# Optimization experiments

Hardware: AMD Instinct MI355X
Metric: run time of the kernel (lower is better)

Reference implementation:

```python
import jax, jax.numpy as jnp
import numpy as np

B, D, H = 65536, 64, 512  # batch, input_dim (even), hidden_dim; num_layers=4 -> 4 Linears


def setup_inputs() -> dict:
    key = jax.random.key(0)
    ks = jax.random.split(key, 10)
    s_in = 1.0 / np.sqrt(D)
    s_h = 1.0 / np.sqrt(H)
    return {
        "t": jnp.zeros((1,), jnp.float32),
        "x": jax.random.normal(ks[0], (B, D), jnp.float32),
        "W0": jax.random.uniform(ks[1], (D, H), jnp.float32, -s_in, s_in),
        "b0": jax.random.uniform(ks[2], (H,), jnp.float32, -s_in, s_in),
        "W1": jax.random.uniform(ks[3], (H, H), jnp.float32, -s_h, s_h),
        "b1": jax.random.uniform(ks[4], (H,), jnp.float32, -s_h, s_h),
        "W2": jax.random.uniform(ks[5], (H, H), jnp.float32, -s_h, s_h),
        "b2": jax.random.uniform(ks[6], (H,), jnp.float32, -s_h, s_h),
        "W3": jax.random.uniform(ks[7], (H, 1), jnp.float32, -s_h, s_h),
        "b3": jax.random.uniform(ks[8], (1,), jnp.float32, -s_h, s_h),
    }


def reference(t, x, W0, b0, W1, b1, W2, b2, W3, b3):
    # Hamiltonian MLP: Linear->Tanh x3, final Linear to scalar energy per sample.
    def hamiltonian_sum(xx):
        h = jnp.tanh(xx @ W0 + b0)
        h = jnp.tanh(h @ W1 + b1)
        h = jnp.tanh(h @ W2 + b2)
        return jnp.sum(h @ W3 + b3)

    gradH = jax.grad(hamiltonian_sum)(x)  # [B, D]
    n = D // 2
    # gradH @ J.T with symplectic J == concat(gradH_p, -gradH_q)
    return jnp.concatenate([gradH[:, n:], -gradH[:, :n]], axis=1)
```

## Files before the change

### kernel.cpp

```cpp
#include <hip/hip_runtime.h>
#include <hip/hip_bf16.h>

typedef unsigned short u16;
typedef short s16x8 __attribute__((ext_vector_type(8)));
typedef float f32x4 __attribute__((ext_vector_type(4)));

#define MFMA_BF16(a, b, c) __builtin_amdgcn_mfma_f32_16x16x32_bf16((a), (b), (c), 0, 0, 0)

static constexpr int D_IN   = 64;
static constexpr int H_DIM  = 512;
static constexpr int M_TILE = 64;
static constexpr int AST    = 520;
static constexpr int XST    = 72;

__device__ __forceinline__ u16 f2bf(float f) {
  unsigned u = __builtin_bit_cast(unsigned, f);
  u += 0x7fffu + ((u >> 16) & 1u);
  return (u16)(u >> 16);
}
__device__ __forceinline__ float bfb2f(unsigned bits16) {
  return __builtin_bit_cast(float, bits16 << 16);
}
__device__ __forceinline__ float fast_tanh(float x) {
  float e = __expf(2.0f * x);
  return 1.0f - 2.0f * __builtin_amdgcn_rcpf(e + 1.0f);
}
#if defined(__gfx950__) && __has_builtin(__builtin_amdgcn_cvt_pk_bf16_f32)
__device__ __forceinline__ unsigned pk2bf(float a, float b) {
  typedef __bf16 bf16x2_t __attribute__((ext_vector_type(2)));
  bf16x2_t v = __builtin_amdgcn_cvt_pk_bf16_f32(a, b);
  return __builtin_bit_cast(unsigned, v);
}
#else
__device__ __forceinline__ unsigned pk2bf(float a, float b) {
  return (unsigned)f2bf(a) | ((unsigned)f2bf(b) << 16);
}
#endif

__global__ void prep_weights(const float* __restrict__ W0,
                             const float* __restrict__ W1,
                             const float* __restrict__ W2,
                             const float* __restrict__ W3,
                             u16* __restrict__ ws) {
  u16* p0f = ws;
  u16* p0b = p0f + D_IN * H_DIM;
  u16* p1f = p0b + D_IN * H_DIM;
  u16* p1b = p1f + H_DIM * H_DIM;
  u16* p2f = p1b + H_DIM * H_DIM;
  u16* p2b = p2f + H_DIM * H_DIM;

  int t = blockIdx.x * 256 + threadIdx.x;
  int lane = t & 63;
  int kc   = (t >> 6) & 15;
  int ntg  = t >> 10;
  int ln = lane & 15, q = lane >> 4;
  int n = ntg * 16 + ln;
  int k = kc * 32 + q * 8;

  #pragma unroll
  for (int j = 0; j < 8; ++j) {
    p1f[t * 8 + j] = f2bf(W1[(k + j) * 512 + n]);
    p2f[t * 8 + j] = f2bf(W2[(k + j) * 512 + n]);
    p1b[t * 8 + j] = f2bf(W1[n * 512 + (k + j)]);
    p2b[t * 8 + j] = f2bf(W2[n * 512 + (k + j)] * W3[k + j]);
  }
  if (kc < 2) {
    int t0 = (ntg * 2 + kc) * 64 + lane;
    #pragma unroll
    for (int j = 0; j < 8; ++j)
      p0f[t0 * 8 + j] = f2bf(W0[(k + j) * 512 + n]);
  }
  if (ntg < 4) {
    int t0 = (ntg * 16 + kc) * 64 + lane;
    #pragma unroll
    for (int j = 0; j < 8; ++j)
      p0b[t0 * 8 + j] = f2bf(W0[n * 512 + (k + j)]);
  }
}

#define LOAD_W4(BP, KC, WA)                                                     \
  {                                                                             \
    const u16* _sr = (BP) + ((size_t)wave << 15) + ((KC) << 9) + lane * 8;      \
    _Pragma("unroll")                                                           \
    for (int s = 0; s < 4; ++s)                                                 \
      (WA)[s] = *(const s16x8*)(_sr + (s << 13));                               \
  }
#define WA_PROLOGUE2(BP)                                                        \
  { LOAD_W4(BP, 0, wa0); LOAD_W4(BP, 1, wa1); }

#define STEP2(KC, WA, BP)                                                       \
  {                                                                             \
    s16x8 b[4];                                                                 \
    _Pragma("unroll")                                                           \
    for (int nt = 0; nt < 4; ++nt)                                              \
      b[nt] = *(const s16x8*)(buf + (nt * 16 + ln) * AST + (KC) * 32 + q * 8);  \
    _Pragma("unroll")                                                           \
    for (int nt = 0; nt < 4; ++nt)                                              \
      _Pragma("unroll")                                                         \
      for (int mt = 0; mt < 4; ++mt)                                            \
        acc[mt][nt] = MFMA_BF16((WA)[mt], b[nt], acc[mt][nt]);                  \
    if ((KC) + 2 < 16) LOAD_W4(BP, (KC) + 2, WA);                               \
  }

#define GEMM512_REG(BP)                                                         \
  {                                                                             \
    STEP2( 0, wa0, BP); STEP2( 1, wa1, BP);                                     \
    STEP2( 2, wa0, BP); STEP2( 3, wa1, BP);                                     \
    STEP2( 4, wa0, BP); STEP2( 5, wa1, BP);                                     \
    STEP2( 6, wa0, BP); STEP2( 7, wa1, BP);                                     \
    STEP2( 8, wa0, BP); STEP2( 9, wa1, BP);                                     \
    STEP2(10, wa0, BP); STEP2(11, wa1, BP);                                     \
    STEP2(12, wa0, BP); STEP2(13, wa1, BP);                                     \
    STEP2(14, wa0, BP); STEP2(15, wa1, BP);                                     \
  }

#define ACC_INIT_BIAS(BIAS)                                                     \
  {                                                                             \
    _Pragma("unroll")                                                           \
    for (int mt = 0; mt < 4; ++mt) {                                            \
      float4 bv = *(const float4*)((BIAS) + wave * 64 + mt * 16 + q * 4);       \
      _Pragma("unroll")                                                         \
      for (int nt = 0; nt < 4; ++nt)                                            \
        acc[mt][nt] = (f32x4){bv.x, bv.y, bv.z, bv.w};                          \
    }                                                                           \
  }
#define ACC_INIT_ZERO()                                                         \
  {                                                                             \
    _Pragma("unroll") for (int mt = 0; mt < 4; ++mt)                            \
      _Pragma("unroll") for (int nt = 0; nt < 4; ++nt)                          \
        acc[mt][nt] = (f32x4){0.f, 0.f, 0.f, 0.f};                              \
  }

__global__ __launch_bounds__(512, 2) void hnn_fused(
    const float* __restrict__ x,
    const float* __restrict__ bias0,
    const float* __restrict__ bias1,
    const float* __restrict__ bias2,
    const u16* __restrict__ ws,
    float* __restrict__ out)
{
  const u16* p0f = ws;
  const u16* p0b = p0f + D_IN * H_DIM;
  const u16* p1f = p0b + D_IN * H_DIM;
  const u16* p1b = p1f + H_DIM * H_DIM;
  const u16* p2f = p1b + H_DIM * H_DIM;
  const u16* p2b = p2f + H_DIM * H_DIM;

  __shared__ __align__(16) u16 xs[M_TILE * XST];
  __shared__ __align__(16) u16 buf[M_TILE * AST];

  const int tid  = threadIdx.x;
  const int wave = tid >> 6;
  const int lane = tid & 63;
  const int ln   = lane & 15;
  const int q    = lane >> 4;
  const int m0   = wave * 64;
  const int row0 = blockIdx.x * M_TILE;

  {
    int r = tid >> 3, c = (tid & 7) * 8;
    const float4* src = (const float4*)(x + (size_t)(row0 + r) * D_IN + c);
    float4 f0 = src[0];
    float4 f1 = src[1];
    u16* dst = xs + r * XST + c;
    dst[0] = f2bf(f0.x); dst[1] = f2bf(f0.y); dst[2] = f2bf(f0.z); dst[3] = f2bf(f0.w);
    dst[4] = f2bf(f1.x); dst[5] = f2bf(f1.y); dst[6] = f2bf(f1.z); dst[7] = f2bf(f1.w);
  }
  __syncthreads();

  f32x4 acc[4][4];
  s16x8 wa0[4], wa1[4];
  unsigned h0p[4][4][2];
  unsigned h1p[4][4][2];

  ACC_INIT_BIAS(bias0);
  {
    const u16* ap0 = p0f + (wave << 12) + lane * 8;
    #pragma unroll
    for (int kc = 0; kc < 2; ++kc) {
      s16x8 b[4];
      #pragma unroll
      for (int nt = 0; nt < 4; ++nt)
        b[nt] = *(const s16x8*)(xs + (nt * 16 + ln) * XST + kc * 32 + q * 8);
      #pragma unroll
      for (int mt = 0; mt < 4; ++mt) {
        s16x8 a = *(const s16x8*)(ap0 + (mt << 10) + (kc << 9));
        #pragma unroll
        for (int nt = 0; nt < 4; ++nt)
          acc[mt][nt] = MFMA_BF16(a, b[nt], acc[mt][nt]);
      }
    }
  }
  WA_PROLOGUE2(p1f);
  #pragma unroll
  for (int mt = 0; mt < 4; ++mt)
    #pragma unroll
    for (int nt = 0; nt < 4; ++nt) {
      unsigned p01 = pk2bf(fast_tanh(acc[mt][nt][0]), fast_tanh(acc[mt][nt][1]));
      unsigned p23 = pk2bf(fast_tanh(acc[mt][nt][2]), fast_tanh(acc[mt][nt][3]));
      h0p[mt][nt][0] = p01; h0p[mt][nt][1] = p23;
      *(uint2*)(buf + (nt * 16 + ln) * AST + m0 + mt * 16 + q * 4) =
          make_uint2(p01, p23);
    }
  __syncthreads();

  ACC_INIT_BIAS(bias1);
  GEMM512_REG(p1f);
  __syncthreads();
  WA_PROLOGUE2(p2f);
  #pragma unroll
  for (int mt = 0; mt < 4; ++mt)
    #pragma unroll
    for (int nt = 0; nt < 4; ++nt) {
      unsigned p01 = pk2bf(fast_tanh(acc[mt][nt][0]), fast_tanh(acc[mt][nt][1]));
      unsigned p23 = pk2bf(fast_tanh(acc[mt][nt][2]), fast_tanh(acc[mt][nt][3]));
      h1p[mt][nt][0] = p01; h1p[mt][nt][1] = p23;
      *(uint2*)(buf + (nt * 16 + ln) * AST + m0 + mt * 16 + q * 4) =
          make_uint2(p01, p23);
    }
  __syncthreads();

  ACC_INIT_BIAS(bias2);
  GEMM512_REG(p2f);
  __syncthreads();
  WA_PROLOGUE2(p2b);
  #pragma unroll
  for (int mt = 0; mt < 4; ++mt)
    #pragma unroll
    for (int nt = 0; nt < 4; ++nt) {
      float t0 = fast_tanh(acc[mt][nt][0]), t1 = fast_tanh(acc[mt][nt][1]);
      float t2 = fast_tanh(acc[mt][nt][2]), t3 = fast_tanh(acc[mt][nt][3]);
      unsigned p01 = pk2bf(1.0f - t0 * t0, 1.0f - t1 * t1);
      unsigned p23 = pk2bf(1.0f - t2 * t2, 1.0f - t3 * t3);
      *(uint2*)(buf + (nt * 16 + ln) * AST + m0 + mt * 16 + q * 4) =
          make_uint2(p01, p23);
    }
  __syncthreads();

  ACC_INIT_ZERO();
  GEMM512_REG(p2b);
  __syncthreads();
  WA_PROLOGUE2(p1b);
  #pragma unroll
  for (int mt = 0; mt < 4; ++mt)
    #pragma unroll
    for (int nt = 0; nt < 4; ++nt) {
      unsigned pa = h1p[mt][nt][0], pb = h1p[mt][nt][1];
      float h0v = bfb2f(pa & 0xffffu), h1v = bfb2f(pa >> 16);
      float h2v = bfb2f(pb & 0xffffu), h3v = bfb2f(pb >> 16);
      unsigned p01 = pk2bf(acc[mt][nt][0] * (1.0f - h0v * h0v),
                           acc[mt][nt][1] * (1.0f - h1v * h1v));
      unsigned p23 = pk2bf(acc[mt][nt][2] * (1.0f - h2v * h2v),
                           acc[mt][nt][3] * (1.0f - h3v * h3v));
      *(uint2*)(buf + (nt * 16 + ln) * AST + m0 + mt * 16 + q * 4) =
          make_uint2(p01, p23);
    }
  __syncthreads();

  ACC_INIT_ZERO();
  GEMM512_REG(p1b);
  __syncthreads();
  #pragma unroll
  for (int mt = 0; mt < 4; ++mt)
    #pragma unroll
    for (int nt = 0; nt < 4; ++nt) {
      unsigned pa = h0p[mt][nt][0], pb = h0p[mt][nt][1];
      float h0v = bfb2f(pa & 0xffffu), h1v = bfb2f(pa >> 16);
      float h2v = bfb2f(pb & 0xffffu), h3v = bfb2f(pb >> 16);
      unsigned p01 = pk2bf(acc[mt][nt][0] * (1.0f - h0v * h0v),
                           acc[mt][nt][1] * (1.0f - h1v * h1v));
      unsigned p23 = pk2bf(acc[mt][nt][2] * (1.0f - h2v * h2v),
                           acc[mt][nt][3] * (1.0f - h3v * h3v));
      *(uint2*)(buf + (nt * 16 + ln) * AST + m0 + mt * 16 + q * 4) =
          make_uint2(p01, p23);
    }
  __syncthreads();

  {
    f32x4 acc5[2];
    acc5[0] = (f32x4){0.f, 0.f, 0.f, 0.f};
    acc5[1] = (f32x4){0.f, 0.f, 0.f, 0.f};
    const int mt5 = wave & 3;
    const int n0  = (wave >> 2) * 32;
    const u16* ap5 = p0b + (mt5 << 13) + lane * 8;
    #pragma unroll 2
    for (int kc = 0; kc < 16; ++kc) {
      s16x8 a = *(const s16x8*)(ap5 + (kc << 9));
      #pragma unroll
      for (int nt = 0; nt < 2; ++nt) {
        s16x8 b = *(const s16x8*)(buf + (n0 + nt * 16 + ln) * AST + kc * 32 + q * 8);
        acc5[nt] = MFMA_BF16(a, b, acc5[nt]);
      }
    }
    int g0 = mt5 * 16 + q * 4;
    int c0 = (g0 < 32) ? g0 + 32 : g0 - 32;
    float s = (g0 < 32) ? -1.0f : 1.0f;
    #pragma unroll
    for (int nt = 0; nt < 2; ++nt) {
      int smp = row0 + n0 + nt * 16 + ln;
      float4 v = make_float4(s * acc5[nt][0], s * acc5[nt][1],
                             s * acc5[nt][2], s * acc5[nt][3]);
      *(float4*)(out + (size_t)smp * 64 + c0) = v;
    }
  }
}

extern "C" void kernel_launch(void* const* d_in, const int* in_sizes, int n_in,
                              void* d_out, int out_size, void* d_ws, size_t ws_size,
                              hipStream_t stream) {
  const float* x  = (const float*)d_in[1];
  const float* W0 = (const float*)d_in[2];
  const float* b0 = (const float*)d_in[3];
  const float* W1 = (const float*)d_in[4];
  const float* b1 = (const float*)d_in[5];
  const float* W2 = (const float*)d_in[6];
  const float* b2 = (const float*)d_in[7];
  const float* W3 = (const float*)d_in[8];
  u16* ws = (u16*)d_ws;
  float* out = (float*)d_out;

  prep_weights<<<128, 256, 0, stream>>>(W0, W1, W2, W3, ws);
  hnn_fused<<<65536 / M_TILE, 512, 0, stream>>>(x, b0, b1, b2, ws, out);
}
```

Before: 244.6 us.

## Double-buffer LDS activations to drop post-GEMM barriers and keep h1 in LDS

The single shared activation buffer becomes two ping-pong LDS buffers. Each layer's epilogue writes into the buffer the just-finished GEMM was not reading, so the __syncthreads after every 512-wide GEMM is removed. The h1 activations are no longer held in registers; they stay in the second LDS buffer and are read back and overwritten in place during the backward step, freeing about 32 VGPRs per thread. The cost is roughly 66 KB more LDS per block, which likely leaves room for only one 512-thread block per CU instead of the two requested by the launch bounds.

Result: faster. 229.2 us (-6.3%).

```diff
diff --git a/kernel.cpp b/kernel.cpp
--- a/kernel.cpp
+++ b/kernel.cpp
@@ -88,12 +88,12 @@
 #define WA_PROLOGUE2(BP)                                                        \
   { LOAD_W4(BP, 0, wa0); LOAD_W4(BP, 1, wa1); }
 
-#define STEP2(KC, WA, BP)                                                       \
+#define STEP2(KC, WA, BP, BUF)                                                  \
   {                                                                             \
     s16x8 b[4];                                                                 \
     _Pragma("unroll")                                                           \
     for (int nt = 0; nt < 4; ++nt)                                              \
-      b[nt] = *(const s16x8*)(buf + (nt * 16 + ln) * AST + (KC) * 32 + q * 8);  \
+      b[nt] = *(const s16x8*)((BUF) + (nt * 16 + ln) * AST + (KC) * 32 + q * 8);\
     _Pragma("unroll")                                                           \
     for (int nt = 0; nt < 4; ++nt)                                              \
       _Pragma("unroll")                                                         \
@@ -102,16 +102,16 @@
     if ((KC) + 2 < 16) LOAD_W4(BP, (KC) + 2, WA);                               \
   }
 
-#define GEMM512_REG(BP)                                                         \
-  {                                                                             \
-    STEP2( 0, wa0, BP); STEP2( 1, wa1, BP);                                     \
-    STEP2( 2, wa0, BP); STEP2( 3, wa1, BP);                                     \
-    STEP2( 4, wa0, BP); STEP2( 5, wa1, BP);                                     \
-    STEP2( 6, wa0, BP); STEP2( 7, wa1, BP);                                     \
-    STEP2( 8, wa0, BP); STEP2( 9, wa1, BP);                                     \
-    STEP2(10, wa0, BP); STEP2(11, wa1, BP);                                     \
-    STEP2(12, wa0, BP); STEP2(13, wa1, BP);                                     \
-    STEP2(14, wa0, BP); STEP2(15, wa1, BP);                                     \
+#define GEMM512_REG(BP, BUF)                                                    \
+  {                                                                             \
+    STEP2( 0, wa0, BP, BUF); STEP2( 1, wa1, BP, BUF);                           \
+    STEP2( 2, wa0, BP, BUF); STEP2( 3, wa1, BP, BUF);                           \
+    STEP2( 4, wa0, BP, BUF); STEP2( 5, wa1, BP, BUF);                           \
+    STEP2( 6, wa0, BP, BUF); STEP2( 7, wa1, BP, BUF);                           \
+    STEP2( 8, wa0, BP, BUF); STEP2( 9, wa1, BP, BUF);                           \
+    STEP2(10, wa0, BP, BUF); STEP2(11, wa1, BP, BUF);                           \
+    STEP2(12, wa0, BP, BUF); STEP2(13, wa1, BP, BUF);                           \
+    STEP2(14, wa0, BP, BUF); STEP2(15, wa1, BP, BUF);                           \
   }
 
 #define ACC_INIT_BIAS(BIAS)                                                     \
@@ -147,7 +147,8 @@
   const u16* p2b = p2f + H_DIM * H_DIM;
 
   __shared__ __align__(16) u16 xs[M_TILE * XST];
-  __shared__ __align__(16) u16 buf[M_TILE * AST];
+  __shared__ __align__(16) u16 bufA[M_TILE * AST];
+  __shared__ __align__(16) u16 bufB[M_TILE * AST];
 
   const int tid  = threadIdx.x;
   const int wave = tid >> 6;
@@ -171,7 +172,6 @@
   f32x4 acc[4][4];
   s16x8 wa0[4], wa1[4];
   unsigned h0p[4][4][2];
-  unsigned h1p[4][4][2];
 
   ACC_INIT_BIAS(bias0);
   {
@@ -199,14 +199,13 @@
       unsigned p01 = pk2bf(fast_tanh(acc[mt][nt][0]), fast_tanh(acc[mt][nt][1]));
       unsigned p23 = pk2bf(fast_tanh(acc[mt][nt][2]), fast_tanh(acc[mt][nt][3]));
       h0p[mt][nt][0] = p01; h0p[mt][nt][1] = p23;
-      *(uint2*)(buf + (nt * 16 + ln) * AST + m0 + mt * 16 + q * 4) =
+      *(uint2*)(bufA + (nt * 16 + ln) * AST + m0 + mt * 16 + q * 4) =
           make_uint2(p01, p23);
     }
   __syncthreads();
 
   ACC_INIT_BIAS(bias1);
-  GEMM512_REG(p1f);
-  __syncthreads();
+  GEMM512_REG(p1f, bufA);
   WA_PROLOGUE2(p2f);
   #pragma unroll
   for (int mt = 0; mt < 4; ++mt)
@@ -214,15 +213,13 @@
     for (int nt = 0; nt < 4; ++nt) {
       unsigned p01 = pk2bf(fast_tanh(acc[mt][nt][0]), fast_tanh(acc[mt][nt][1]));
       unsigned p23 = pk2bf(fast_tanh(acc[mt][nt][2]), fast_tanh(acc[mt][nt][3]));
-      h1p[mt][nt][0] = p01; h1p[mt][nt][1] = p23;
-      *(uint2*)(buf + (nt * 16 + ln) * AST + m0 + mt * 16 + q * 4) =
+      *(uint2*)(bufB + (nt * 16 + ln) * AST + m0 + mt * 16 + q * 4) =
           make_uint2(p01, p23);
     }
   __syncthreads();
 
   ACC_INIT_BIAS(bias2);
-  GEMM512_REG(p2f);
-  __syncthreads();
+  GEMM512_REG(p2f, bufB);
   WA_PROLOGUE2(p2b);
   #pragma unroll
   for (int mt = 0; mt < 4; ++mt)
@@ -232,34 +229,32 @@
       float t2 = fast_tanh(acc[mt][nt][2]), t3 = fast_tanh(acc[mt][nt][3]);
       unsigned p01 = pk2bf(1.0f - t0 * t0, 1.0f - t1 * t1);
       unsigned p23 = pk2bf(1.0f - t2 * t2, 1.0f - t3 * t3);
-      *(uint2*)(buf + (nt * 16 + ln) * AST + m0 + mt * 16 + q * 4) =
+      *(uint2*)(bufA + (nt * 16 + ln) * AST + m0 + mt * 16 + q * 4) =
           make_uint2(p01, p23);
     }
   __syncthreads();
 
   ACC_INIT_ZERO();
-  GEMM512_REG(p2b);
-  __syncthreads();
+  GEMM512_REG(p2b, bufA);
   WA_PROLOGUE2(p1b);
   #pragma unroll
   for (int mt = 0; mt < 4; ++mt)
     #pragma unroll
     for (int nt = 0; nt < 4; ++nt) {
-      unsigned pa = h1p[mt][nt][0], pb = h1p[mt][nt][1];
-      float h0v = bfb2f(pa & 0xffffu), h1v = bfb2f(pa >> 16);
-      float h2v = bfb2f(pb & 0xffffu), h3v = bfb2f(pb >> 16);
+      uint2* hp = (uint2*)(bufB + (nt * 16 + ln) * AST + m0 + mt * 16 + q * 4);
+      uint2 hv = *hp;
+      float h0v = bfb2f(hv.x & 0xffffu), h1v = bfb2f(hv.x >> 16);
+      float h2v = bfb2f(hv.y & 0xffffu), h3v = bfb2f(hv.y >> 16);
       unsigned p01 = pk2bf(acc[mt][nt][0] * (1.0f - h0v * h0v),
                            acc[mt][nt][1] * (1.0f - h1v * h1v));
       unsigned p23 = pk2bf(acc[mt][nt][2] * (1.0f - h2v * h2v),
                            acc[mt][nt][3] * (1.0f - h3v * h3v));
-      *(uint2*)(buf + (nt * 16 + ln) * AST + m0 + mt * 16 + q * 4) =
-          make_uint2(p01, p23);
+      *hp = make_uint2(p01, p23);
     }
   __syncthreads();
 
   ACC_INIT_ZERO();
-  GEMM512_REG(p1b);
-  __syncthreads();
+  GEMM512_REG(p1b, bufB);
   #pragma unroll
   for (int mt = 0; mt < 4; ++mt)
     #pragma unroll
@@ -271,7 +266,7 @@
                            acc[mt][nt][1] * (1.0f - h1v * h1v));
       unsigned p23 = pk2bf(acc[mt][nt][2] * (1.0f - h2v * h2v),
                            acc[mt][nt][3] * (1.0f - h3v * h3v));
-      *(uint2*)(buf + (nt * 16 + ln) * AST + m0 + mt * 16 + q * 4) =
+      *(uint2*)(bufA + (nt * 16 + ln) * AST + m0 + mt * 16 + q * 4) =
           make_uint2(p01, p23);
     }
   __syncthreads();
@@ -288,7 +283,7 @@
       s16x8 a = *(const s16x8*)(ap5 + (kc << 9));
       #pragma unroll
       for (int nt = 0; nt < 2; ++nt) {
-        s16x8 b = *(const s16x8*)(buf + (n0 + nt * 16 + ln) * AST + kc * 32 + q * 8);
+        s16x8 b = *(const s16x8*)(bufA + (n0 + nt * 16 + ln) * AST + kc * 32 + q * 8);
         acc5[nt] = MFMA_BF16(a, b, acc5[nt]);
       }
     }
```
